# Kernel tuning notes

Measured on AMD Instinct MI355X. Metric: run time of the kernel, lower is better.

Reference implementation:

```python
import jax, jax.numpy as jnp
import numpy as np

NOISE_DB = 40.0  # layer's `noise` ctor arg (SNR in dB)


def setup_inputs() -> dict:
    key = jax.random.key(0)
    k1, k2, k3 = jax.random.split(key, 3)
    B, M, L, S = 4, 256, 24, 22  # S = shots = round(M*L/(M+L-1))
    x = jax.random.normal(k1, (B, M, M, L), dtype=jnp.float32)
    # coded aperture weights, init N(0,1)/sqrt(kern*kern) as in build()
    H = jax.random.normal(k2, (1, M, M, 1, S), dtype=jnp.float32) / np.float32(M)
    # standard-normal noise sample (the layer draws this internally)
    noise_eps = jax.random.normal(k3, (B, M, M + L - 1, 1), dtype=jnp.float32)
    return {"x": x, "H": H, "noise_eps": noise_eps}


def reference(x, H, noise_eps):
    B, M, _, L = x.shape
    S = H.shape[-1]
    W = M + L - 1  # dispersed detector width
    H2 = H[0, :, :, 0, :]  # (M, M, S)

    # Aux1 = H * x : (B, M, M, L, S)
    HX = H2[None, :, :, None, :] * x[..., None]

    # Forward shear-sum: Y[b,m,n,s] = sum_i HX[b,m,n-i,i,s]
    # (equivalent to the pad + L rolls + extract-band-i + reduce_sum)
    Y = jnp.zeros((B, M, W, S), dtype=x.dtype)
    for i in range(L):  # fixed small spectral loop; indexed accumulation, no padded rolls
        Y = Y.at[:, :, i:i + M, :].add(HX[:, :, :, i, :])

    # Noise: sigma^2 = ||Y||^2 / (M * W * B * 10^(noise/10)); broadcast over shots
    sigm = jnp.sum(Y * Y) / (M * W * B * (10.0 ** (NOISE_DB / 10.0)))
    Y = Y + jnp.sqrt(sigm) * noise_eps  # noise_eps: (B, M, W, 1)

    # Reverse shift-extract: X[b,m,n,i] = sum_s H2[m,n,s] * Y[b,m,n+i,s]
    Ys = jnp.stack([Y[:, :, i:i + M, :] for i in range(L)], axis=3)  # (B,M,M,L,S)
    X = jnp.einsum('bmnls,mns->bmnl', Ys, H2)

    return X / jnp.max(X)
```

## Files before the change

kernel.cpp:

```cpp
#include <hip/hip_runtime.h>
#include <math.h>

namespace {
constexpr int Mz = 256, Lz = 24, Sz = 22, Bz = 4;
constexpr int Wz = Mz + Lz - 1;
constexpr int ST = 26;
constexpr int XT = 257;
constexpr int NBLK = Bz * Mz;
constexpr double SIGM_DEN = (double)Mz * (double)Wz * (double)Bz * 1e4;
}

__device__ __forceinline__ unsigned int enc_f32(float f) {
  unsigned int u = __float_as_uint(f);
  return (u & 0x80000000u) ? ~u : (u | 0x80000000u);
}
__device__ __forceinline__ float dec_f32(unsigned int e) {
  unsigned int u = (e & 0x80000000u) ? (e ^ 0x80000000u) : ~e;
  return __uint_as_float(u);
}

__global__ __launch_bounds__(256) void k_init(const float* __restrict__ H,
                                              float* __restrict__ hsum,
                                              double* __restrict__ sumsq,
                                              unsigned int* __restrict__ maxenc)
{
  int idx = blockIdx.x * 256 + threadIdx.x;
  if (idx == 0) { *sumsq = 0.0; *maxenc = 0u; }
  if (idx < Mz * Mz) {
    const float* __restrict__ hp = H + (size_t)idx * Sz;
    float a = 0.f;
    #pragma unroll
    for (int s = 0; s < Sz; ++s) a += hp[s];
    hsum[idx] = a;
  }
}

__global__ __launch_bounds__(256) void k_fwd(const float* __restrict__ x,
                                             const float* __restrict__ H,
                                             float* __restrict__ X0,
                                             double* __restrict__ sumsq)
{
  __shared__ __align__(16) float Hs[Mz * ST];
  __shared__ __align__(16) float Ys[Wz * ST];
  __shared__ __align__(16) float xs[Lz * XT];
  __shared__ double wred[4];

  const int tid = threadIdx.x;
  const int b = blockIdx.x >> 8;
  const int m = blockIdx.x & 255;
  const float* __restrict__ xp = x + (size_t)(b * Mz + m) * (Mz * Lz);
  const float* __restrict__ Hp = H + (size_t)m * (Mz * Sz);

  for (int e = tid; e < Mz * Sz; e += 256) {
    int n = e / Sz, s = e - n * Sz;
    Hs[n * ST + s] = Hp[e];
  }
  for (int e = tid; e < Mz * Lz; e += 256) {
    int n = e / Lz, i = e - n * Lz;
    xs[i * XT + n] = xp[e];
  }
  __syncthreads();

  double local = 0.0;
  for (int w = tid; w < Wz; w += 256) {
    const int i0 = (w > Mz - 1) ? (w - (Mz - 1)) : 0;
    const int i1 = (w < Lz - 1) ? w : (Lz - 1);
    float2 acc[11];
    #pragma unroll
    for (int k = 0; k < 11; ++k) acc[k] = make_float2(0.f, 0.f);
    for (int i = i0; i <= i1; ++i) {
      const int n = w - i;
      const float xv = xs[i * XT + n];
      const float2* __restrict__ hrow = (const float2*)&Hs[n * ST];
      #pragma unroll
      for (int k = 0; k < 11; ++k) {
        const float2 h = hrow[k];
        acc[k].x = fmaf(h.x, xv, acc[k].x);
        acc[k].y = fmaf(h.y, xv, acc[k].y);
      }
    }
    float2* __restrict__ yrow = (float2*)&Ys[w * ST];
    #pragma unroll
    for (int k = 0; k < 11; ++k) {
      yrow[k] = acc[k];
      local += (double)acc[k].x * acc[k].x + (double)acc[k].y * acc[k].y;
    }
  }

  for (int off = 32; off > 0; off >>= 1) local += __shfl_down(local, off, 64);
  const int lane = tid & 63, wid = tid >> 6;
  if (lane == 0) wred[wid] = local;
  __syncthreads();
  if (tid == 0) atomicAdd(sumsq, wred[0] + wred[1] + wred[2] + wred[3]);

  {
    const int n = tid;
    float hr[Sz];
    {
      const float2* __restrict__ h2 = (const float2*)&Hs[n * ST];
      #pragma unroll
      for (int k = 0; k < 11; ++k) { const float2 h = h2[k]; hr[2*k] = h.x; hr[2*k+1] = h.y; }
    }
    float4* __restrict__ Xp4 =
        (float4*)(X0 + (size_t)(b * Mz + m) * (Mz * Lz) + n * Lz);
    #pragma unroll
    for (int q = 0; q < 6; ++q) {
      float o[4];
      #pragma unroll
      for (int j = 0; j < 4; ++j) {
        const int l = 4 * q + j;
        const float2* __restrict__ yr = (const float2*)&Ys[(n + l) * ST];
        float a0 = 0.f, a1 = 0.f;
        #pragma unroll
        for (int k = 0; k < 11; ++k) {
          const float2 y = yr[k];
          a0 = fmaf(y.x, hr[2*k],   a0);
          a1 = fmaf(y.y, hr[2*k+1], a1);
        }
        o[j] = a0 + a1;
      }
      Xp4[q] = make_float4(o[0], o[1], o[2], o[3]);
    }
  }
}

__global__ __launch_bounds__(256) void k_max(const float* __restrict__ X0,
                                             const float* __restrict__ eps,
                                             const float* __restrict__ hsum,
                                             const double* __restrict__ sumsq,
                                             unsigned int* __restrict__ maxenc)
{
  const float c = sqrtf((float)(*sumsq / SIGM_DEN));
  const int n = threadIdx.x;
  const int bm = blockIdx.x;
  const int m = bm & 255;
  const float4* __restrict__ r4 = (const float4*)(X0 + (size_t)bm * (Mz * Lz) + n * Lz);
  const float* __restrict__ ep = eps + bm * Wz + n;
  const float hv = c * hsum[(m << 8) + n];

  float mx = -3.4e38f;
  #pragma unroll
  for (int q = 0; q < 6; ++q) {
    float4 t = r4[q];
    mx = fmaxf(mx, fmaf(hv, ep[4*q+0], t.x));
    mx = fmaxf(mx, fmaf(hv, ep[4*q+1], t.y));
    mx = fmaxf(mx, fmaf(hv, ep[4*q+2], t.z));
    mx = fmaxf(mx, fmaf(hv, ep[4*q+3], t.w));
  }
  for (int off = 32; off > 0; off >>= 1) mx = fmaxf(mx, __shfl_down(mx, off, 64));
  __shared__ float wredf[4];
  const int lane = n & 63, wid = n >> 6;
  if (lane == 0) wredf[wid] = mx;
  __syncthreads();
  if (n == 0) {
    float bmx = fmaxf(fmaxf(wredf[0], wredf[1]), fmaxf(wredf[2], wredf[3]));
    atomicMax(maxenc, enc_f32(bmx));
  }
}

__global__ __launch_bounds__(256) void k_final(float* __restrict__ Xio,
                                               const float* __restrict__ eps,
                                               const float* __restrict__ hsum,
                                               const double* __restrict__ sumsq,
                                               const unsigned int* __restrict__ maxenc)
{
  const float c = sqrtf((float)(*sumsq / SIGM_DEN));
  const float inv = 1.0f / dec_f32(*maxenc);
  const int n = threadIdx.x;
  const int bm = blockIdx.x;
  const int m = bm & 255;
  float4* __restrict__ r4 = (float4*)(Xio + (size_t)bm * (Mz * Lz) + n * Lz);
  const float* __restrict__ ep = eps + bm * Wz + n;
  const float hv = c * hsum[(m << 8) + n];

  #pragma unroll
  for (int q = 0; q < 6; ++q) {
    float4 t = r4[q];
    t.x = fmaf(hv, ep[4*q+0], t.x) * inv;
    t.y = fmaf(hv, ep[4*q+1], t.y) * inv;
    t.z = fmaf(hv, ep[4*q+2], t.z) * inv;
    t.w = fmaf(hv, ep[4*q+3], t.w) * inv;
    r4[q] = t;
  }
}

extern "C" void kernel_launch(void* const* d_in, const int* in_sizes, int n_in,
                              void* d_out, int out_size, void* d_ws, size_t ws_size,
                              hipStream_t stream) {
  const float* x   = (const float*)d_in[0];
  const float* H   = (const float*)d_in[1];
  const float* eps = (const float*)d_in[2];
  float* out = (float*)d_out;

  double*       sumsq  = (double*)d_ws;
  unsigned int* maxenc = (unsigned int*)((char*)d_ws + 8);
  float*        hsum   = (float*)((char*)d_ws + 16);

  k_init  <<<(Mz * Mz + 255) / 256, 256, 0, stream>>>(H, hsum, sumsq, maxenc);
  k_fwd   <<<NBLK, 256, 0, stream>>>(x, H, out, sumsq);
  k_max   <<<NBLK, 256, 0, stream>>>(out, eps, hsum, sumsq, maxenc);
  k_final <<<NBLK, 256, 0, stream>>>(out, eps, hsum, sumsq, maxenc);
}
```

Before: 135.9 us.

## Compute forward shear-sum in registers with DPP lane shifts instead of LDS staging

The forward dispersion sum no longer stages H and x in shared memory. Each wave loads one H row and one x row per lane straight into registers. It accumulates all shots and shifts the partial sums down one lane per spectral band with DPP wave shifts, producing 41 output columns per 64-lane pass with a 23-lane halo. This cuts shared memory use so more blocks fit per CU (launch bounds now request 4) and removes the LDS transpose stores. The cost is redundant halo work, an uneven split of 7 passes across 4 waves, and strided global loads for H and x.

```diff
diff --git a/kernel.cpp b/kernel.cpp
--- a/kernel.cpp
+++ b/kernel.cpp
@@ -5,8 +5,8 @@
 constexpr int Mz = 256, Lz = 24, Sz = 22, Bz = 4;
 constexpr int Wz = Mz + Lz - 1;
 constexpr int ST = 26;
-constexpr int XT = 257;
 constexpr int NBLK = Bz * Mz;
+constexpr int NPASS = 7;
 constexpr double SIGM_DEN = (double)Mz * (double)Wz * (double)Bz * 1e4;
 }
 
@@ -17,6 +17,11 @@
 __device__ __forceinline__ float dec_f32(unsigned int e) {
   unsigned int u = (e & 0x80000000u) ? (e ^ 0x80000000u) : ~e;
   return __uint_as_float(u);
+}
+
+__device__ __forceinline__ float rot_down1(float v) {
+  return __int_as_float(
+      __builtin_amdgcn_update_dpp(0, __float_as_int(v), 0x130, 0xF, 0xF, true));
 }
 
 __global__ __launch_bounds__(256) void k_init(const float* __restrict__ H,
@@ -35,55 +40,71 @@
   }
 }
 
-__global__ __launch_bounds__(256) void k_fwd(const float* __restrict__ x,
-                                             const float* __restrict__ H,
-                                             float* __restrict__ X0,
-                                             double* __restrict__ sumsq)
-{
-  __shared__ __align__(16) float Hs[Mz * ST];
+__global__ __launch_bounds__(256, 4) void k_fwd(const float* __restrict__ x,
+                                                const float* __restrict__ H,
+                                                float* __restrict__ X0,
+                                                double* __restrict__ sumsq)
+{
   __shared__ __align__(16) float Ys[Wz * ST];
-  __shared__ __align__(16) float xs[Lz * XT];
   __shared__ double wred[4];
 
   const int tid = threadIdx.x;
+  const int j  = tid & 63;
+  const int wv = tid >> 6;
   const int b = blockIdx.x >> 8;
   const int m = blockIdx.x & 255;
   const float* __restrict__ xp = x + (size_t)(b * Mz + m) * (Mz * Lz);
   const float* __restrict__ Hp = H + (size_t)m * (Mz * Sz);
 
-  for (int e = tid; e < Mz * Sz; e += 256) {
-    int n = e / Sz, s = e - n * Sz;
-    Hs[n * ST + s] = Hp[e];
-  }
-  for (int e = tid; e < Mz * Lz; e += 256) {
-    int n = e / Lz, i = e - n * Lz;
-    xs[i * XT + n] = xp[e];
-  }
-  __syncthreads();
-
   double local = 0.0;
-  for (int w = tid; w < Wz; w += 256) {
-    const int i0 = (w > Mz - 1) ? (w - (Mz - 1)) : 0;
-    const int i1 = (w < Lz - 1) ? w : (Lz - 1);
-    float2 acc[11];
-    #pragma unroll
-    for (int k = 0; k < 11; ++k) acc[k] = make_float2(0.f, 0.f);
-    for (int i = i0; i <= i1; ++i) {
-      const int n = w - i;
-      const float xv = xs[i * XT + n];
-      const float2* __restrict__ hrow = (const float2*)&Hs[n * ST];
+
+  for (int pp = 0; pp < 2; ++pp) {
+    const int p = wv + 4 * pp;
+    if (p >= NPASS) break;
+    const int W0 = 41 * p;
+    const int n = W0 - 23 + j;
+    const bool valid = (n >= 0) && (n < Mz);
+
+    float hr[Sz], xr[Lz];
+    if (valid) {
+      const float2* __restrict__ h2 = (const float2*)(Hp + n * Sz);
+      #pragma unroll
+      for (int k = 0; k < 11; ++k) { const float2 h = h2[k]; hr[2*k] = h.x; hr[2*k+1] = h.y; }
+      const float4* __restrict__ x4 = (const float4*)(xp + n * Lz);
+      #pragma unroll
+      for (int k = 0; k < 6; ++k) {
+        const float4 t = x4[k];
+        xr[4*k] = t.x; xr[4*k+1] = t.y; xr[4*k+2] = t.z; xr[4*k+3] = t.w;
+      }
+    } else {
+      #pragma unroll
+      for (int k = 0; k < Sz; ++k) hr[k] = 0.f;
+      #pragma unroll
+      for (int k = 0; k < Lz; ++k) xr[k] = 0.f;
+    }
+
+    float acc[Sz];
+    #pragma unroll
+    for (int s = 0; s < Sz; ++s) acc[s] = 0.f;
+
+    #pragma unroll
+    for (int i = 0; i < Lz; ++i) {
+      #pragma unroll
+      for (int s = 0; s < Sz; ++s) acc[s] = fmaf(hr[s], xr[i], acc[s]);
+      if (i < Lz - 1) {
+        #pragma unroll
+        for (int s = 0; s < Sz; ++s) acc[s] = rot_down1(acc[s]);
+      }
+    }
+
+    const int w = W0 + j;
+    if (j <= 40 && w < Wz) {
+      float2* __restrict__ yrow = (float2*)&Ys[w * ST];
       #pragma unroll
       for (int k = 0; k < 11; ++k) {
-        const float2 h = hrow[k];
-        acc[k].x = fmaf(h.x, xv, acc[k].x);
-        acc[k].y = fmaf(h.y, xv, acc[k].y);
-      }
-    }
-    float2* __restrict__ yrow = (float2*)&Ys[w * ST];
-    #pragma unroll
-    for (int k = 0; k < 11; ++k) {
-      yrow[k] = acc[k];
-      local += (double)acc[k].x * acc[k].x + (double)acc[k].y * acc[k].y;
+        yrow[k] = make_float2(acc[2*k], acc[2*k+1]);
+        local += (double)acc[2*k] * acc[2*k] + (double)acc[2*k+1] * acc[2*k+1];
+      }
     }
   }
 
@@ -97,7 +118,7 @@
     const int n = tid;
     float hr[Sz];
     {
-      const float2* __restrict__ h2 = (const float2*)&Hs[n * ST];
+      const float2* __restrict__ h2 = (const float2*)(Hp + n * Sz);
       #pragma unroll
       for (int k = 0; k < 11; ++k) { const float2 h = h2[k]; hr[2*k] = h.x; hr[2*k+1] = h.y; }
     }
@@ -107,8 +128,8 @@
     for (int q = 0; q < 6; ++q) {
       float o[4];
       #pragma unroll
-      for (int j = 0; j < 4; ++j) {
-        const int l = 4 * q + j;
+      for (int jj = 0; jj < 4; ++jj) {
+        const int l = 4 * q + jj;
         const float2* __restrict__ yr = (const float2*)&Ys[(n + l) * ST];
         float a0 = 0.f, a1 = 0.f;
         #pragma unroll
@@ -117,7 +138,7 @@
           a0 = fmaf(y.x, hr[2*k],   a0);
           a1 = fmaf(y.y, hr[2*k+1], a1);
         }
-        o[j] = a0 + a1;
+        o[jj] = a0 + a1;
       }
       Xp4[q] = make_float4(o[0], o[1], o[2], o[3]);
     }
```

After: 129.4 us. 4.8% less time.
